# Optimization experiments

Measured on AMD Instinct MI355X. Metric: run time of the kernel, lower is better.

## Reference

```python
import jax, jax.numpy as jnp
from jax import lax
import numpy as np

DIM = 768        # d_model (mamba-130m)
D_IN = 1024      # vision encoder feature dim
NQ = 384         # num_queries
NB = 12          # num_blocks
BATCH = 2
LSEQ = 1024      # image tokens
DI = 2 * DIM     # mamba d_inner (expand=2)
DS = 16          # d_state
DC = 4           # d_conv
DTR = 48         # dt_rank = ceil(768/16)
NH = 16          # attention heads
HD = DIM // NH
NM = NB + 2      # mamba instances: fwd-enc, bwd-enc, one per block


def _ln(x, g, b):
    m = jnp.mean(x, -1, keepdims=True)
    v = jnp.mean((x - m) ** 2, -1, keepdims=True)
    return (x - m) * lax.rsqrt(v + 1e-5) * g + b


def _mamba(x, in_w, conv_w, conv_b, xproj_w, dt_w, dt_b, A_log, Dp, out_w):
    # x: (B, L, DIM)
    Bb = x.shape[0]
    xz = x @ in_w.T                      # (B, L, 2*DI)
    xi, z = jnp.split(xz, 2, -1)
    # depthwise causal conv1d over time
    xc = lax.conv_general_dilated(xi.transpose(0, 2, 1), conv_w[:, None, :], (1,),
                                  [(DC - 1, 0)], feature_group_count=DI,
                                  dimension_numbers=('NCH', 'OIH', 'NCH'))
    xc = jax.nn.silu((xc + conv_b[None, :, None]).transpose(0, 2, 1))  # (B, L, DI)
    dbl = xc @ xproj_w.T                 # (B, L, DTR + 2*DS)
    dt, Bm, Cm = jnp.split(dbl, [DTR, DTR + DS], -1)
    dt = jax.nn.softplus(dt @ dt_w.T + dt_b)   # (B, L, DI)
    A = -jnp.exp(A_log)                        # (DI, DS)
    dA = jnp.exp(dt[..., None] * A)            # (B, L, DI, DS)
    dBx = dt[..., None] * Bm[:, :, None, :] * xc[..., None]

    def step(h, inp):
        dA_t, dBx_t, C_t = inp
        h = dA_t * h + dBx_t
        return h, jnp.einsum('bds,bs->bd', h, C_t)

    h0 = jnp.zeros((Bb, DI, DS), x.dtype)
    _, ys = lax.scan(step, h0, (dA.transpose(1, 0, 2, 3), dBx.transpose(1, 0, 2, 3), Cm.transpose(1, 0, 2)))
    y = ys.transpose(1, 0, 2) + Dp * xc
    y = y * jax.nn.silu(z)
    return y @ out_w.T


def _local_allowed(nq, nk):
    # matches Attention.get_local_mask: query i attends to its contiguous key block
    kpq, extra = nk // nq, nk % nq
    i = jnp.arange(nq)
    start = i * kpq + jnp.minimum(i, extra)
    end = start + kpq + (i < extra)
    k = jnp.arange(nk)
    return (k[None, :] >= start[:, None]) & (k[None, :] < end[:, None])


def _mha(q_in, kv, in_w, in_b, out_w, out_b, allowed):
    # nn.MultiheadAttention(dim, 16, batch_first=True) cross-attention
    wq, wk, wv = jnp.split(in_w, 3, 0)
    bq, bk, bv = jnp.split(in_b, 3, 0)
    Bb = q_in.shape[0]
    q = (q_in @ wq.T + bq).reshape(Bb, -1, NH, HD)
    k = (kv @ wk.T + bk).reshape(Bb, -1, NH, HD)
    v = (kv @ wv.T + bv).reshape(Bb, -1, NH, HD)
    s = jnp.einsum('bqhd,bkhd->bhqk', q, k) / np.float32(np.sqrt(HD))
    s = jnp.where(allowed[None, None], s, -jnp.inf)
    a = jax.nn.softmax(s, -1)
    o = jnp.einsum('bhqk,bkhd->bqhd', a, v).reshape(Bb, -1, DIM)
    return o @ out_w.T + out_b


def _model(img_emb, queries, vision_proj_w, vision_proj_b, ln_vision_g, ln_vision_b,
           mamba_in_w, mamba_conv_w, mamba_conv_b, mamba_xproj_w, mamba_dt_w, mamba_dt_b,
           mamba_A_log, mamba_D, mamba_out_w, seq_norm_g, seq_norm_b,
           attn_in_w, attn_in_b, attn_out_w, attn_out_b, cross_w, cross_b):
    mp = lambda i: (mamba_in_w[i], mamba_conv_w[i], mamba_conv_b[i], mamba_xproj_w[i],
                    mamba_dt_w[i], mamba_dt_b[i], mamba_A_log[i], mamba_D[i], mamba_out_w[i])
    feats = _ln(img_emb @ vision_proj_w.T + vision_proj_b, ln_vision_g, ln_vision_b)
    fwd = _mamba(feats, *mp(0))
    bwd = jnp.flip(_mamba(jnp.flip(feats, 1), *mp(1)), 1)
    c = fwd + bwd + feats
    x = jnp.broadcast_to(queries, (img_emb.shape[0], NQ, DIM))
    allowed = _local_allowed(NQ, c.shape[1])
    for l in range(NB):
        x = _ln(x, seq_norm_g[l], seq_norm_b[l])
        x = _mamba(x, *mp(l + 2)) + x
        score = _mha(x, c, attn_in_w[l], attn_in_b[l], attn_out_w[l], attn_out_b[l], allowed)
        x = jnp.concatenate([x, score], -1) @ cross_w[l].T + cross_b[l]
    return x


_model_jit = jax.jit(_model)


def setup_inputs() -> dict:
    key = jax.random.key(0)
    ks = iter(jax.random.split(key, 24))
    rn = lambda shape, s=0.02: jax.random.normal(next(ks), shape, jnp.float32) * s
    A_log = jnp.broadcast_to(jnp.log(jnp.arange(1, DS + 1, dtype=jnp.float32)), (NM, DI, DS))
    return {
        'img_emb': rn((BATCH, LSEQ, D_IN), 1.0),
        'queries': rn((1, NQ, DIM)),
        'vision_proj_w': rn((DIM, D_IN)),
        'vision_proj_b': jnp.zeros((DIM,), jnp.float32),
        'ln_vision_g': jnp.ones((DIM,), jnp.float32),
        'ln_vision_b': jnp.zeros((DIM,), jnp.float32),
        'mamba_in_w': rn((NM, 2 * DI, DIM)),
        'mamba_conv_w': rn((NM, DI, DC), 0.1),
        'mamba_conv_b': jnp.zeros((NM, DI), jnp.float32),
        'mamba_xproj_w': rn((NM, DTR + 2 * DS, DI)),
        'mamba_dt_w': rn((NM, DI, DTR), 0.1),
        'mamba_dt_b': rn((NM, DI), 0.5),
        'mamba_A_log': A_log,
        'mamba_D': jnp.ones((NM, DI), jnp.float32),
        'mamba_out_w': rn((NM, DIM, DI)),
        'seq_norm_g': jnp.ones((NB, DIM), jnp.float32),
        'seq_norm_b': jnp.zeros((NB, DIM), jnp.float32),
        'attn_in_w': rn((NB, 3 * DIM, DIM)),
        'attn_in_b': jnp.zeros((NB, 3 * DIM), jnp.float32),
        'attn_out_w': rn((NB, DIM, DIM)),
        'attn_out_b': jnp.zeros((NB, DIM), jnp.float32),
        'cross_w': rn((NB, DIM, 2 * DIM)),
        'cross_b': jnp.zeros((NB, DIM), jnp.float32),
    }


def reference(img_emb, queries, vision_proj_w, vision_proj_b, ln_vision_g, ln_vision_b,
              mamba_in_w, mamba_conv_w, mamba_conv_b, mamba_xproj_w, mamba_dt_w, mamba_dt_b,
              mamba_A_log, mamba_D, mamba_out_w, seq_norm_g, seq_norm_b,
              attn_in_w, attn_in_b, attn_out_w, attn_out_b, cross_w, cross_b):
    return _model_jit(img_emb, queries, vision_proj_w, vision_proj_b, ln_vision_g, ln_vision_b,
                      mamba_in_w, mamba_conv_w, mamba_conv_b, mamba_xproj_w, mamba_dt_w, mamba_dt_b,
                      mamba_A_log, mamba_D, mamba_out_w, seq_norm_g, seq_norm_b,
                      attn_in_w, attn_in_b, attn_out_w, attn_out_b, cross_w, cross_b)
```

## Files before the change

kernel.cpp:

```cpp
#include <hip/hip_runtime.h>
#include <hip/hip_bf16.h>

#define DIMQ 768
#define D_IN 1024
#define NQ 384
#define NBK 12
#define BATCH 2
#define LSEQ 1024
#define DI 1536
#define DS 16
#define DTR 48
#define NH 16
#define HD 48

typedef __attribute__((ext_vector_type(8))) short short8;
typedef __attribute__((ext_vector_type(4))) float f32x4;

#define GF_BIAS 1
#define GF_SOFTPLUS 2
#define EPI_BIAS 1
#define EPI_ADDT 2

#define LOG2E 1.4426950408889634f

__device__ __forceinline__ unsigned short f2bf(float f) {
    unsigned int u = __builtin_bit_cast(unsigned int, f);
    u = (u + 0x7FFFu + ((u >> 16) & 1u)) >> 16;
    return (unsigned short)u;
}
__device__ __forceinline__ float bf2f(unsigned short h) {
    unsigned int u = ((unsigned int)h) << 16;
    return __builtin_bit_cast(float, u);
}

__device__ __forceinline__ void gload_lds16(const void* g, void* l) {
    __builtin_amdgcn_global_load_lds(
        (const __attribute__((address_space(1))) void*)g,
        (__attribute__((address_space(3))) void*)l, 16, 0, 0);
}

struct WTab {
    const float* src[10];
    long long dstOff[10];
    long long ps[10];
    int cum[10];
    int rows[10], cols[10], dcols[10];
    int n;
    int total;
};

__global__ void wconv_kernel(unsigned short* __restrict__ dst, WTab T)
{
    const int i = blockIdx.x * 256 + threadIdx.x;
    if (i >= T.total) return;
    int sI = 0;
    while (i >= T.cum[sI]) ++sI;
    const int e = i - (sI ? T.cum[sI - 1] : 0);
    const int dcols = T.dcols[sI];
    const int r = e / dcols;
    const int c = e - r * dcols;
    float v = 0.f;
    if (r < T.rows[sI] && c < T.cols[sI]) v = T.src[sI][(long long)r * T.cols[sI] + c];
    const unsigned short h = f2bf(v);
    const unsigned short l = f2bf(v - bf2f(h));
    dst[T.dstOff[sI] + e] = h;
    dst[T.dstOff[sI] + T.ps[sI] + e] = l;
}

struct LTab {
    const float* src[7];
    long long srcStride[7], dstOff[7], ps[7];
    int rows[7], cols[7], dcols[7], cum[7];
};

__global__ __launch_bounds__(256)
void wconv_layers(unsigned short* __restrict__ dst, long long layerStride, int lBase, LTab T)
{
    const int e = blockIdx.x * 256 + threadIdx.x;
    const int l = blockIdx.y + lBase;
    int sI = 0;
    while (e >= T.cum[sI]) ++sI;
    const int eo = e - (sI ? T.cum[sI - 1] : 0);
    const int dc = T.dcols[sI];
    const int r = eo / dc;
    const int c = eo - r * dc;
    float v = 0.f;
    if (r < T.rows[sI] && c < T.cols[sI])
        v = T.src[sI][(long long)l * T.srcStride[sI] + (long long)r * T.cols[sI] + c];
    const unsigned short h = f2bf(v);
    const unsigned short lo2 = f2bf(v - bf2f(h));
    unsigned short* d = dst + (long long)blockIdx.y * layerStride + T.dstOff[sI];
    d[eo] = h;
    d[T.ps[sI] + eo] = lo2;
}

__global__ __launch_bounds__(256, 3)
void gemm_direct(const float* __restrict__ Ag, const unsigned short* __restrict__ Bhl,
                 float* __restrict__ Cg, const float* __restrict__ biasg,
                 int M, int N, int K, int lda, int ldb, int ldc,
                 long long sA, long long sB, long long sC, long long sBias,
                 long long planeB, int flags)
{
    __shared__ __align__(16) unsigned short As[2][2][64][40];
    __shared__ __align__(16) unsigned short Bs[2][2][128][32];

    const int z = blockIdx.z;
    const float* A = Ag + (size_t)z * sA;
    const unsigned short* Bhi = Bhl + (size_t)z * sB;
    const unsigned short* Blo = Bhi + planeB;
    float* C = Cg + (size_t)z * sC;

    const int mBase = blockIdx.x * 64;
    const int nBase = blockIdx.y * 128;
    const int tid = threadIdx.x, lane = tid & 63, wave = tid >> 6;
    const int lm = lane & 15, lq = lane >> 4;
    const int wn = wave * 32;
    const int arow = tid >> 2, aq = tid & 3;
    const int brow = lane >> 2;
    const int bcol = (lane & 3) * 8;

    const int ktiles = (K + 31) >> 5;

    auto issueB = [&](int t, int buf) {
#pragma unroll
        for (int cc = 0; cc < 4; ++cc) {
            const int chunk = wave * 4 + cc;
            const int pl = chunk >> 3;
            const int r16 = chunk & 7;
            const unsigned short* bp = pl ? Blo : Bhi;
            const int n = nBase + r16 * 16 + brow;
            gload_lds16(bp + (size_t)n * ldb + t * 32 + bcol, &Bs[buf][pl][r16 * 16][0]);
        }
    };
    auto loadA = [&](int t, float* v) {
        const int col = t * 32 + aq * 8;
        const float* src = A + (size_t)(mBase + arow) * lda + col;
#pragma unroll
        for (int u = 0; u < 2; ++u) {
            float4 t4 = make_float4(0.f, 0.f, 0.f, 0.f);
            if (col + u * 4 < K) t4 = *(const float4*)(src + u * 4);
            v[u*4+0]=t4.x; v[u*4+1]=t4.y; v[u*4+2]=t4.z; v[u*4+3]=t4.w;
        }
    };
    auto writeA = [&](const float* v, int buf) {
        short8 ph, plv;
#pragma unroll
        for (int j = 0; j < 8; ++j) {
            unsigned short h = f2bf(v[j]);
            ph[j] = (short)h;
            plv[j] = (short)f2bf(v[j] - bf2f(h));
        }
        *(short8*)&As[buf][0][arow][aq * 8] = ph;
        *(short8*)&As[buf][1][arow][aq * 8] = plv;
    };

    float av[8];
    issueB(0, 0);
    loadA(0, av);
    writeA(av, 0);

    f32x4 acc[4][2] = {};
    for (int t = 0; t < ktiles; ++t) {
        const int buf = t & 1;
        __syncthreads();
        const bool more = (t + 1) < ktiles;
        if (more) { issueB(t + 1, buf ^ 1); loadA(t + 1, av); }
        short8 ah[4], al[4], bh[2], bl[2];
#pragma unroll
        for (int i = 0; i < 4; ++i) {
            ah[i] = *(const short8*)&As[buf][0][16*i + lm][lq * 8];
            al[i] = *(const short8*)&As[buf][1][16*i + lm][lq * 8];
        }
#pragma unroll
        for (int j = 0; j < 2; ++j) {
            bh[j] = *(const short8*)&Bs[buf][0][wn + 16*j + lm][lq * 8];
            bl[j] = *(const short8*)&Bs[buf][1][wn + 16*j + lm][lq * 8];
        }
#pragma unroll
        for (int i = 0; i < 4; ++i)
#pragma unroll
            for (int j = 0; j < 2; ++j) {
                acc[i][j] = __builtin_amdgcn_mfma_f32_16x16x32_bf16(ah[i], bh[j], acc[i][j], 0, 0, 0);
                acc[i][j] = __builtin_amdgcn_mfma_f32_16x16x32_bf16(ah[i], bl[j], acc[i][j], 0, 0, 0);
                acc[i][j] = __builtin_amdgcn_mfma_f32_16x16x32_bf16(al[i], bh[j], acc[i][j], 0, 0, 0);
            }
        if (more) writeA(av, buf ^ 1);
    }

#pragma unroll
    for (int i = 0; i < 4; ++i)
#pragma unroll
        for (int j = 0; j < 2; ++j)
#pragma unroll
            for (int r = 0; r < 4; ++r) {
                const int m = mBase + i*16 + lq*4 + r;
                const int n = nBase + wn + j*16 + lm;
                float v = acc[i][j][r];
                if (flags & GF_BIAS)     v += biasg[(size_t)z * sBias + n];
                if (flags & GF_SOFTPLUS) v = (v > 20.f) ? v : log1pf(expf(v));
                C[(size_t)m * ldc + n] = v;
            }
}

__global__ __launch_bounds__(256, 3)
void gemm_splitk(const float* __restrict__ Ag, const unsigned short* __restrict__ Bhl,
                 float* __restrict__ Cp,
                 int M, int kLen, int S, int lda, int ldb, int ldP,
                 long long sA, long long sB, long long planeB)
{
    __shared__ __align__(16) unsigned short As[2][2][64][40];
    __shared__ __align__(16) unsigned short Bs[2][2][128][32];

    const int bz = blockIdx.z;
    const int s = bz % S, z = bz / S;
    const int kOff = s * kLen;
    const float* A = Ag + (size_t)z * sA;
    const unsigned short* Bhi = Bhl + (size_t)z * sB;
    const unsigned short* Blo = Bhi + planeB;

    const int mBase = blockIdx.x * 64;
    const int nBase = blockIdx.y * 128;
    const int tid = threadIdx.x, lane = tid & 63, wave = tid >> 6;
    const int lm = lane & 15, lq = lane >> 4;
    const int wn = wave * 32;
    const int arow = tid >> 2, aq = tid & 3;
    const int brow = lane >> 2;
    const int bcol = (lane & 3) * 8;

    const int ktiles = kLen >> 5;

    auto issueB = [&](int t, int buf) {
#pragma unroll
        for (int cc = 0; cc < 4; ++cc) {
            const int chunk = wave * 4 + cc;
            const int pl = chunk >> 3;
            const int r16 = chunk & 7;
            const unsigned short* bp = pl ? Blo : Bhi;
            const int n = nBase + r16 * 16 + brow;
            gload_lds16(bp + (size_t)n * ldb + kOff + t * 32 + bcol, &Bs[buf][pl][r16 * 16][0]);
        }
    };
    auto loadA = [&](int t, float* v) {
        const float* src = A + (size_t)(mBase + arow) * lda + kOff + t * 32 + aq * 8;
#pragma unroll
        for (int u = 0; u < 2; ++u) {
            const float4 t4 = *(const float4*)(src + u * 4);
            v[u*4+0]=t4.x; v[u*4+1]=t4.y; v[u*4+2]=t4.z; v[u*4+3]=t4.w;
        }
    };
    auto writeA = [&](const float* v, int buf) {
        short8 ph, plv;
#pragma unroll
        for (int j = 0; j < 8; ++j) {
            unsigned short h = f2bf(v[j]);
            ph[j] = (short)h;
            plv[j] = (short)f2bf(v[j] - bf2f(h));
        }
        *(short8*)&As[buf][0][arow][aq * 8] = ph;
        *(short8*)&As[buf][1][arow][aq * 8] = plv;
    };

    float av[8];
    issueB(0, 0);
    loadA(0, av);
    writeA(av, 0);

    f32x4 acc[4][2] = {};
    for (int t = 0; t < ktiles; ++t) {
        const int buf = t & 1;
        __syncthreads();
        const bool more = (t + 1) < ktiles;
        if (more) { issueB(t + 1, buf ^ 1); loadA(t + 1, av); }
        short8 ah[4], al[4], bh[2], bl[2];
#pragma unroll
        for (int i = 0; i < 4; ++i) {
            ah[i] = *(const short8*)&As[buf][0][16*i + lm][lq * 8];
            al[i] = *(const short8*)&As[buf][1][16*i + lm][lq * 8];
        }
#pragma unroll
        for (int j = 0; j < 2; ++j) {
            bh[j] = *(const short8*)&Bs[buf][0][wn + 16*j + lm][lq * 8];
            bl[j] = *(const short8*)&Bs[buf][1][wn + 16*j + lm][lq * 8];
        }
#pragma unroll
        for (int i = 0; i < 4; ++i)
#pragma unroll
            for (int j = 0; j < 2; ++j) {
                acc[i][j] = __builtin_amdgcn_mfma_f32_16x16x32_bf16(ah[i], bh[j], acc[i][j], 0, 0, 0);
                acc[i][j] = __builtin_amdgcn_mfma_f32_16x16x32_bf16(ah[i], bl[j], acc[i][j], 0, 0, 0);
                acc[i][j] = __builtin_amdgcn_mfma_f32_16x16x32_bf16(al[i], bh[j], acc[i][j], 0, 0, 0);
            }
        if (more) writeA(av, buf ^ 1);
    }

    float* Cb = Cp + (size_t)bz * M * ldP;
#pragma unroll
    for (int i = 0; i < 4; ++i)
#pragma unroll
        for (int j = 0; j < 2; ++j)
#pragma unroll
            for (int r = 0; r < 4; ++r) {
                const int m = mBase + i*16 + lq*4 + r;
                const int n = nBase + wn + j*16 + lm;
                Cb[(size_t)m * ldP + n] = acc[i][j][r];
            }
}

__global__ void epi_kernel(const float* __restrict__ Cp, float* __restrict__ outF,
                           const float* __restrict__ bias, const float* __restrict__ addT,
                           int Z, int S, int M, int N, int ldP, int ldOut,
                           long long sOutZ, long long sBiasZ, int ldAdd, int flags)
{
    const int n4 = N >> 2;
    const int idx = blockIdx.x * 256 + threadIdx.x;
    if (idx >= Z * M * n4) return;
    const int c4 = idx % n4;
    const int rem = idx / n4;
    const int m = rem % M;
    const int z = rem / M;
    const int n = c4 * 4;
    const float* base = Cp + ((size_t)z * S * M + m) * ldP + n;
    float4 v = *(const float4*)base;
    for (int s = 1; s < S; ++s) {
        const float4 u = *(const float4*)(base + (size_t)s * M * ldP);
        v.x += u.x; v.y += u.y; v.z += u.z; v.w += u.w;
    }
    if (flags & EPI_BIAS) {
        const float4 b4 = *(const float4*)(bias + (size_t)z * sBiasZ + n);
        v.x += b4.x; v.y += b4.y; v.z += b4.z; v.w += b4.w;
    }
    if (flags & EPI_ADDT) {
        const float4 a4 = *(const float4*)(addT + (size_t)m * ldAdd + n);
        v.x += a4.x; v.y += a4.y; v.z += a4.z; v.w += a4.w;
    }
    *(float4*)(outF + (size_t)z * sOutZ + (size_t)m * ldOut + n) = v;
}

__global__ void ln_kernel(const float* __restrict__ in, float* __restrict__ out,
                          const float* __restrict__ g, const float* __restrict__ b,
                          int rows, int srcMod)
{
    const int row = blockIdx.x * 4 + (threadIdx.x >> 6);
    const int lane = threadIdx.x & 63;
    if (row >= rows) return;
    const float* p = in + (size_t)(row % srcMod) * DIMQ;
    float v[12], s = 0.f, s2 = 0.f;
#pragma unroll
    for (int j = 0; j < 12; ++j) {
        v[j] = p[j*64 + lane];
        s += v[j];
        s2 += v[j]*v[j];
    }
#pragma unroll
    for (int o = 32; o; o >>= 1) { s += __shfl_xor(s, o); s2 += __shfl_xor(s2, o); }
    const float mean = s * (1.f/768.f);
    const float var  = s2 * (1.f/768.f) - mean*mean;
    const float inv  = rsqrtf(var + 1e-5f);
    float* q = out + (size_t)row * DIMQ;
#pragma unroll
    for (int j = 0; j < 12; ++j) {
        const int c = j*64 + lane;
        q[c] = (v[j] - mean) * inv * g[c] + b[c];
    }
}

__global__ void conv_kernel(const float* __restrict__ xz, float* __restrict__ xc,
                            const float* __restrict__ cw, const float* __restrict__ cb,
                            int Bn, int L, int instShift)
{
    const int idx = blockIdx.x * 256 + threadIdx.x;
    const int total = Bn * L * (DI/4);
    if (idx >= total) return;
    const int d4 = idx % (DI/4);
    const int t  = (idx / (DI/4)) % L;
    const int b  = idx / (L * (DI/4));
    const int inst = b >> instShift;
    const int d = d4 * 4;
    const float* base = xz + (size_t)(b * L) * 3072 + d;
    const float4 w0 = *(const float4*)(cw + (size_t)(inst*DI + d + 0) * 4);
    const float4 w1 = *(const float4*)(cw + (size_t)(inst*DI + d + 1) * 4);
    const float4 w2 = *(const float4*)(cw + (size_t)(inst*DI + d + 2) * 4);
    const float4 w3 = *(const float4*)(cw + (size_t)(inst*DI + d + 3) * 4);
    float4 acc = *(const float4*)(cb + (size_t)inst*DI + d);
    float4 xv[4];
#pragma unroll
    for (int j = 0; j < 4; ++j) {
        const int tt = t - 3 + j;
        xv[j] = (tt >= 0) ? *(const float4*)(base + (size_t)tt * 3072) : make_float4(0,0,0,0);
    }
    acc.x += xv[0].x*w0.x + xv[1].x*w0.y + xv[2].x*w0.z + xv[3].x*w0.w;
    acc.y += xv[0].y*w1.x + xv[1].y*w1.y + xv[2].y*w1.z + xv[3].y*w1.w;
    acc.z += xv[0].z*w2.x + xv[1].z*w2.y + xv[2].z*w2.z + xv[3].z*w2.w;
    acc.w += xv[0].w*w3.x + xv[1].w*w3.y + xv[2].w*w3.z + xv[3].w*w3.w;
    float4 o;
    o.x = acc.x / (1.f + expf(-acc.x));
    o.y = acc.y / (1.f + expf(-acc.y));
    o.z = acc.z / (1.f + expf(-acc.z));
    o.w = acc.w / (1.f + expf(-acc.w));
    *(float4*)(xc + (size_t)(b * L + t) * DI + d) = o;
}

__global__ __launch_bounds__(256)
void scan_p1(const float* __restrict__ dt, const float* __restrict__ dbl,
             const float* __restrict__ xc, const float* __restrict__ A_log,
             float* __restrict__ hend, float* __restrict__ sumdt,
             int L, int CL, int Bn, int instShift)
{
    const int d = blockIdx.x * 256 + threadIdx.x;
    const int b = blockIdx.y;
    const int c = blockIdx.z;
    const int inst = b >> instShift;
    const float* ap = A_log + ((size_t)inst * DI + d) * DS;
    float A2[16];
#pragma unroll
    for (int s = 0; s < 16; ++s) A2[s] = -expf(ap[s]) * LOG2E;
    float h[16] = {};
    float sd = 0.f;
    const int t0 = c * CL;
    const size_t rowbase = (size_t)b * L;
    for (int t = t0; t < t0 + CL; ++t) {
        const size_t row = rowbase + t;
        const float dtv = dt[row * DI + d];
        const float xcv = xc[row * DI + d];
        float Bv[16];
        *(float4*)(Bv + 0)  = *(const float4*)(dbl + row * 80 + 48);
        *(float4*)(Bv + 4)  = *(const float4*)(dbl + row * 80 + 52);
        *(float4*)(Bv + 8)  = *(const float4*)(dbl + row * 80 + 56);
        *(float4*)(Bv + 12) = *(const float4*)(dbl + row * 80 + 60);
        sd += dtv;
        const float bx = dtv * xcv;
#pragma unroll
        for (int s = 0; s < 16; ++s)
            h[s] = exp2f(dtv * A2[s]) * h[s] + bx * Bv[s];
    }
    float* hp = hend + (((size_t)c * Bn + b) * DI + d) * DS;
#pragma unroll
    for (int s = 0; s < 16; s += 4)
        *(float4*)(hp + s) = make_float4(h[s], h[s+1], h[s+2], h[s+3]);
    sumdt[((size_t)c * Bn + b) * DI + d] = sd;
}

__global__ void scan_p2(const float* __restrict__ hend, const float* __restrict__ sumdt,
                        const float* __restrict__ A_log, float* __restrict__ hstart,
                        int NC, int Bn, int instShift)
{
    const int gid = blockIdx.x * 256 + threadIdx.x;
    const int s = gid & 15;
    const int rem = gid >> 4;
    const int d = rem % DI;
    const int b = rem / DI;
    const int inst = b >> instShift;
    const float A2 = -expf(A_log[((size_t)inst * DI + d) * DS + s]) * LOG2E;
    float carry = 0.f;
    for (int c = 0; c < NC; ++c) {
        const size_t off = (((size_t)c * Bn + b) * DI + d) * DS + s;
        hstart[off] = carry;
        carry = exp2f(A2 * sumdt[((size_t)c * Bn + b) * DI + d]) * carry + hend[off];
    }
}

__global__ __launch_bounds__(256)
void scan_p3(const float* __restrict__ dt, const float* __restrict__ dbl,
             const float* __restrict__ xc, const float* __restrict__ xz,
             const float* __restrict__ A_log, const float* __restrict__ Dp,
             const float* __restrict__ hstart, float* __restrict__ y,
             int L, int CL, int Bn, int instShift)
{
    const int d = blockIdx.x * 256 + threadIdx.x;
    const int b = blockIdx.y;
    const int c = blockIdx.z;
    const int inst = b >> instShift;
    const float* ap = A_log + ((size_t)inst * DI + d) * DS;
    float A2[16];
#pragma unroll
    for (int s = 0; s < 16; ++s) A2[s] = -expf(ap[s]) * LOG2E;
    const float Dd = Dp[(size_t)inst * DI + d];
    float h[16];
    const float* hp = hstart + (((size_t)c * Bn + b) * DI + d) * DS;
#pragma unroll
    for (int s = 0; s < 16; s += 4) {
        const float4 t4 = *(const float4*)(hp + s);
        h[s] = t4.x; h[s+1] = t4.y; h[s+2] = t4.z; h[s+3] = t4.w;
    }
    const int t0 = c * CL;
    const size_t rowbase = (size_t)b * L;
    for (int t = t0; t < t0 + CL; ++t) {
        const size_t row = rowbase + t;
        const float dtv = dt[row * DI + d];
        const float xcv = xc[row * DI + d];
        const float zv  = xz[row * 3072 + DI + d];
        float Bv[16], Cv[16];
        *(float4*)(Bv + 0)  = *(const float4*)(dbl + row * 80 + 48);
        *(float4*)(Bv + 4)  = *(const float4*)(dbl + row * 80 + 52);
        *(float4*)(Bv + 8)  = *(const float4*)(dbl + row * 80 + 56);
        *(float4*)(Bv + 12) = *(const float4*)(dbl + row * 80 + 60);
        *(float4*)(Cv + 0)  = *(const float4*)(dbl + row * 80 + 64);
        *(float4*)(Cv + 4)  = *(const float4*)(dbl + row * 80 + 68);
        *(float4*)(Cv + 8)  = *(const float4*)(dbl + row * 80 + 72);
        *(float4*)(Cv + 12) = *(const float4*)(dbl + row * 80 + 76);
        const float bx = dtv * xcv;
#pragma unroll
        for (int s = 0; s < 16; ++s)
            h[s] = exp2f(dtv * A2[s]) * h[s] + bx * Bv[s];
        float p0 = 0.f, p1 = 0.f, p2 = 0.f, p3 = 0.f;
#pragma unroll
        for (int s = 0; s < 4; ++s) {
            p0 += h[s]      * Cv[s];
            p1 += h[s + 4]  * Cv[s + 4];
            p2 += h[s + 8]  * Cv[s + 8];
            p3 += h[s + 12] * Cv[s + 12];
        }
        const float p = (p0 + p1) + (p2 + p3);
        y[row * DI + d] = (p + Dd * xcv) * (zv / (1.f + expf(-zv)));
    }
}

__global__ void attn_kernel(const float* __restrict__ q, const float* __restrict__ kv,
                            float* __restrict__ o)
{
    const int bi = blockIdx.x;
    const int b = bi / NQ, i = bi % NQ;
    const int tid = threadIdx.x;
    const int h = tid >> 2, r = tid & 3;
    int start, len;
    if (i < 256) { start = 3*i; len = 3; } else { start = 2*i + 256; len = 2; }
    const float* qp = q + (size_t)bi * DIMQ + h*48 + r*12;
    float qv[12];
#pragma unroll
    for (int u = 0; u < 12; ++u) qv[u] = qp[u];
    float s[3] = {-1e30f, -1e30f, -1e30f};
    for (int j = 0; j < len; ++j) {
        const float* kp = kv + (size_t)(b*LSEQ + start + j) * 1536 + h*48 + r*12;
        float p = 0.f;
#pragma unroll
        for (int u = 0; u < 12; ++u) p += qv[u] * kp[u];
        p += __shfl_xor(p, 1);
        p += __shfl_xor(p, 2);
        s[j] = p * 0.14433756729740644f;
    }
    const float mx = fmaxf(s[0], fmaxf(s[1], s[2]));
    float e[3];
    e[0] = expf(s[0]-mx); e[1] = expf(s[1]-mx); e[2] = expf(s[2]-mx);
    const float inv = 1.f / (e[0] + e[1] + e[2]);
    float ov[12] = {};
    for (int j = 0; j < len; ++j) {
        const float w = e[j] * inv;
        const float* vp = kv + (size_t)(b*LSEQ + start + j) * 1536 + 768 + h*48 + r*12;
#pragma unroll
        for (int u = 0; u < 12; ++u) ov[u] += w * vp[u];
    }
    float* op = o + (size_t)bi * DIMQ + h*48 + r*12;
#pragma unroll
    for (int u = 0; u < 12; ++u) op[u] = ov[u];
}

__global__ void flip_kernel(float* __restrict__ X2)
{
    const int idx = blockIdx.x * 256 + threadIdx.x;
    if (idx >= 2*1024*192) return;
    const int d4 = idx % 192;
    const int t  = (idx / 192) % 1024;
    const int b  = idx / (192 * 1024);
    const size_t dst = ((size_t)((2+b)*1024 + t)) * DIMQ + d4*4;
    const size_t src = ((size_t)(b*1024 + (1023 - t))) * DIMQ + d4*4;
    *(float4*)(X2 + dst) = *(const float4*)(X2 + src);
}

__global__ void combine_kernel(const float* __restrict__ oe, const float* __restrict__ feats,
                               float* __restrict__ c)
{
    const int idx = blockIdx.x * 256 + threadIdx.x;
    if (idx >= 2*1024*192) return;
    const int d4 = idx % 192;
    const int t  = (idx / 192) % 1024;
    const int b  = idx / (192 * 1024);
    const size_t fw = ((size_t)(b*1024 + t)) * DIMQ + d4*4;
    const size_t bw = ((size_t)((2+b)*1024 + (1023 - t))) * DIMQ + d4*4;
    const float4 a = *(const float4*)(oe + fw);
    const float4 bb = *(const float4*)(oe + bw);
    const float4 f = *(const float4*)(feats + fw);
    float4 o;
    o.x = a.x + bb.x + f.x; o.y = a.y + bb.y + f.y;
    o.z = a.z + bb.z + f.z; o.w = a.w + bb.w + f.w;
    *(float4*)(c + fw) = o;
}

extern "C" void kernel_launch(void* const* d_in, const int* in_sizes, int n_in,
                              void* d_out, int out_size, void* d_ws, size_t ws_size,
                              hipStream_t stream) {
    const float* img_emb  = (const float*)d_in[0];
    const float* queries  = (const float*)d_in[1];
    const float* vis_w    = (const float*)d_in[2];
    const float* vis_b    = (const float*)d_in[3];
    const float* lnv_g    = (const float*)d_in[4];
    const float* lnv_b    = (const float*)d_in[5];
    const float* m_in_w   = (const float*)d_in[6];
    const float* m_conv_w = (const float*)d_in[7];
    const float* m_conv_b = (const float*)d_in[8];
    const float* m_xp_w   = (const float*)d_in[9];
    const float* m_dt_w   = (const float*)d_in[10];
    const float* m_dt_b   = (const float*)d_in[11];
    const float* m_A_log  = (const float*)d_in[12];
    const float* m_D      = (const float*)d_in[13];
    const float* m_out_w  = (const float*)d_in[14];
    const float* sn_g     = (const float*)d_in[15];
    const float* sn_b     = (const float*)d_in[16];
    const float* a_in_w   = (const float*)d_in[17];
    const float* a_in_b   = (const float*)d_in[18];
    const float* a_out_w  = (const float*)d_in[19];
    const float* a_out_b  = (const float*)d_in[20];
    const float* cr_w     = (const float*)d_in[21];
    const float* cr_b     = (const float*)d_in[22];
    float* out = (float*)d_out;

    float* ws = (float*)d_ws;
    auto alloc = [&](size_t n) { float* p = ws; ws += n; return p; };
    float* X2   = alloc((size_t)4096*768);
    float* xzb  = alloc((size_t)4096*3072);
    float* xcb  = alloc((size_t)4096*1536);
    float* dblb = alloc((size_t)4096*80);
    float* dtb  = alloc((size_t)4096*1536);
    float* yb   = alloc((size_t)4096*1536);
    float* oe   = alloc((size_t)4096*768);
    float* cbuf = alloc((size_t)2048*768);
    float* xbuf = alloc((size_t)768*768);
    float* xn   = alloc((size_t)768*768);
    float* x1s  = alloc((size_t)768*1536);
    float* qb   = alloc((size_t)768*768);
    float* ob   = alloc((size_t)768*768);
    float* Cp   = alloc((size_t)2359296);
    unsigned short* wenc = (unsigned short*)alloc((size_t)16908288/2);

    const long long LAYER_USH = 14745600;
    const size_t usedFloats = (size_t)(ws - (float*)d_ws);
    const size_t needFull = (usedFloats + (size_t)12 * (LAYER_USH/2)) * 4;
    const bool bigW = ws_size >= needFull;
    unsigned short* wlayAll = (unsigned short*)ws;

    const long long P_VIS = 768LL*1024;
    const long long P_IN  = 3072LL*768;
    const long long P_XP  = 128LL*1536;
    const long long P_DT  = 1536LL*64;
    const long long P_OUT = 768LL*1536;
    const long long P_AIN = 2304LL*768;
    const long long P_AOUT= 768LL*768;
    const long long P_CR  = 768LL*1536;
    const long long off_vis   = 0;
    const long long off_encIn = 2*P_VIS;
    const long long off_encXp = off_encIn + 4*P_IN;
    const long long off_encDt = off_encXp + 4*P_XP;
    const long long off_encOut= off_encDt + 4*P_DT;
    const long long off_in  = 0;
    const long long off_xp  = 2*P_IN;
    const long long off_dt  = off_xp + 2*P_XP;
    const long long off_out = off_dt + 2*P_DT;
    const long long off_aIn = off_out + 2*P_OUT;
    const long long off_aOut= off_aIn + 2*P_AIN;
    const long long off_cr  = off_aOut + 2*P_AOUT;

    auto addSeg = [](WTab& T, const float* src, int rows, int cols, int drows, int dcols,
                     long long dstOff) {
        const int k = T.n;
        T.src[k] = src; T.rows[k] = rows; T.cols[k] = cols; T.dcols[k] = dcols;
        T.ps[k] = (long long)drows * dcols;
        T.dstOff[k] = dstOff;
        T.total += drows * dcols;
        T.cum[k] = T.total;
        T.n = k + 1;
    };

    auto GD = [&](const float* A, const unsigned short* Bhl, long long planeB,
                  float* C, const float* bias,
                  int M, int N, int K, int lda, int ldb, int ldc,
                  long long sA, long long sB, long long sC, long long sBias,
                  int Z, int flags) {
        dim3 grid(M/64, N/128, Z);
        gemm_direct<<<grid, 256, 0, stream>>>(A, Bhl, C, bias, M, N, K, lda, ldb, ldc,
                                              sA, sB, sC, sBias, planeB, flags);
    };
    auto GS = [&](const float* A, const unsigned short* Bhl, long long planeB,
                  int M, int Ntile, int kLen, int S, int lda, int ldb, int ldP,
                  long long sA, long long sB, int Z) {
        dim3 grid(M/64, Ntile/128, Z*S);
        gemm_splitk<<<grid, 256, 0, stream>>>(A, Bhl, Cp, M, kLen, S, lda, ldb, ldP,
                                              sA, sB, planeB);
    };
    auto EPI = [&](float* outF, const float* bias, const float* addT,
                   int Z, int S, int M, int N, int ldP, int ldOut,
                   long long sOutZ, long long sBiasZ, int ldAdd, int flags) {
        const int total = Z * M * (N/4);
        epi_kernel<<<(total+255)/256, 256, 0, stream>>>(Cp, outF, bias, addT, Z, S, M, N,
                                                        ldP, ldOut, sOutZ, sBiasZ, ldAdd, flags);
    };

    {
        WTab T = {}; T.n = 0; T.total = 0;
        addSeg(T, vis_w, 768, 1024, 768, 1024, off_vis);
        addSeg(T, m_in_w,               3072, 768, 3072, 768, off_encIn);
        addSeg(T, m_in_w + 3072*768,    3072, 768, 3072, 768, off_encIn + 2*P_IN);
        addSeg(T, m_xp_w,               80, 1536, 128, 1536, off_encXp);
        addSeg(T, m_xp_w + 80*1536,     80, 1536, 128, 1536, off_encXp + 2*P_XP);
        addSeg(T, m_dt_w,               1536, 48, 1536, 64, off_encDt);
        addSeg(T, m_dt_w + 1536*48,     1536, 48, 1536, 64, off_encDt + 2*P_DT);
        addSeg(T, m_out_w,              768, 1536, 768, 1536, off_encOut);
        addSeg(T, m_out_w + 768*1536,   768, 1536, 768, 1536, off_encOut + 2*P_OUT);
        wconv_kernel<<<(T.total+255)/256, 256, 0, stream>>>(wenc, T);
    }

    LTab LT = {};
    {
        auto seg = [&](int k, const float* src, long long srcStride, int rows, int cols,
                       int drows, int dcols, long long dstOff) {
            LT.src[k] = src; LT.srcStride[k] = srcStride;
            LT.rows[k] = rows; LT.cols[k] = cols; LT.dcols[k] = dcols;
            LT.ps[k] = (long long)drows * dcols; LT.dstOff[k] = dstOff;
            LT.cum[k] = (k ? LT.cum[k-1] : 0) + drows * dcols;
        };
        seg(0, m_in_w  + (size_t)2*3072*768, 3072LL*768, 3072, 768, 3072, 768, off_in);
        seg(1, m_xp_w  + (size_t)2*80*1536,  80LL*1536,  80, 1536, 128, 1536, off_xp);
        seg(2, m_dt_w  + (size_t)2*1536*48,  1536LL*48,  1536, 48, 1536, 64, off_dt);
        seg(3, m_out_w + (size_t)2*768*1536, 768LL*1536, 768, 1536, 768, 1536, off_out);
        seg(4, a_in_w,  2304LL*768, 2304, 768, 2304, 768, off_aIn);
        seg(5, a_out_w, 768LL*768,  768, 768, 768, 768, off_aOut);
        seg(6, cr_w,    768LL*1536, 768, 1536, 768, 1536, off_cr);
    }
    if (bigW)
        wconv_layers<<<dim3(28800, 12), 256, 0, stream>>>(wlayAll, LAYER_USH, 0, LT);

    GD(img_emb, wenc + off_vis, P_VIS, oe, vis_b,
       2048, 768, 1024, 1024, 1024, 768, 0,0,0,0, 1, GF_BIAS);
    ln_kernel<<<512, 256, 0, stream>>>(oe, X2, lnv_g, lnv_b, 2048, 2048);
    flip_kernel<<<(2*1024*192 + 255)/256, 256, 0, stream>>>(X2);

    GD(X2, wenc + off_encIn, P_IN, xzb, nullptr,
       2048, 3072, 768, 768, 768, 3072, 2048LL*768, 2*P_IN, 2048LL*3072, 0, 2, 0);
    conv_kernel<<<(4*1024*384 + 255)/256, 256, 0, stream>>>(xzb, xcb, m_conv_w, m_conv_b, 4, 1024, 1);
    GS(xcb, wenc + off_encXp, P_XP, 2048, 128, 384, 4, 1536, 1536, 128,
       2048LL*1536, 2*P_XP, 2);
    EPI(dblb, nullptr, nullptr, 2, 4, 2048, 80, 128, 80, 2048LL*80, 0, 0, 0);
    GD(dblb, wenc + off_encDt, P_DT, dtb, m_dt_b,
       2048, 1536, 48, 80, 64, 1536, 2048LL*80, 2*P_DT, 2048LL*1536, 1536, 2,
       GF_BIAS | GF_SOFTPLUS);
    {
        const int NC = 16, CL = 64;
        float* hend   = oe;
        float* hstart = oe + (size_t)NC*4*DI*DS;
        float* sumdt  = cbuf;
        scan_p1<<<dim3(6, 4, NC), 256, 0, stream>>>(dtb, dblb, xcb, m_A_log, hend, sumdt, 1024, CL, 4, 1);
        scan_p2<<<(4*DI*DS)/256, 256, 0, stream>>>(hend, sumdt, m_A_log, hstart, NC, 4, 1);
        scan_p3<<<dim3(6, 4, NC), 256, 0, stream>>>(dtb, dblb, xcb, xzb, m_A_log, m_D, hstart, yb, 1024, CL, 4, 1);
    }
    GD(yb, wenc + off_encOut, P_OUT, oe, nullptr,
       2048, 768, 1536, 1536, 1536, 768, 2048LL*1536, 2*P_OUT, 2048LL*768, 0, 2, 0);
    combine_kernel<<<(2*1024*192 + 255)/256, 256, 0, stream>>>(oe, X2, cbuf);

    for (int l = 0; l < NBK; ++l) {
        const int li = l + 2;
        const unsigned short* wl = bigW ? wlayAll + (size_t)l * LAYER_USH : wlayAll;
        if (!bigW)
            wconv_layers<<<dim3(28800, 1), 256, 0, stream>>>((unsigned short*)wlayAll, LAYER_USH, l, LT);

        ln_kernel<<<192, 256, 0, stream>>>(l == 0 ? queries : xbuf, xn,
                                           sn_g + (size_t)l*768, sn_b + (size_t)l*768,
                                           768, l == 0 ? 384 : 768);
        GD(xn, wl + off_in, P_IN, xzb, nullptr,
           768, 3072, 768, 768, 768, 3072, 0,0,0,0, 1, 0);
        conv_kernel<<<(2*NQ*384 + 255)/256, 256, 0, stream>>>(
            xzb, xcb, m_conv_w + (size_t)li*DI*4, m_conv_b + (size_t)li*DI, 2, NQ, 8);
        GS(xcb, wl + off_xp, P_XP, 768, 128, 96, 16, 1536, 1536, 128, 0, 0, 1);
        EPI(dblb, nullptr, nullptr, 1, 16, 768, 80, 128, 80, 0, 0, 0, 0);
        GD(dblb, wl + off_dt, P_DT, dtb, m_dt_b + (size_t)li*1536,
           768, 1536, 48, 80, 64, 1536, 0,0,0,0, 1, GF_BIAS | GF_SOFTPLUS);
        {
            const int NC = 24, CL = 16;
            const float* Ap = m_A_log + (size_t)li*DI*DS;
            float* hend   = oe;
            float* hstart = oe + (size_t)NC*2*DI*DS;
            float* sumdt  = oe + (size_t)2*NC*2*DI*DS;
            scan_p1<<<dim3(6, 2, NC), 256, 0, stream>>>(dtb, dblb, xcb, Ap, hend, sumdt, NQ, CL, 2, 8);
            scan_p2<<<(2*DI*DS)/256, 256, 0, stream>>>(hend, sumdt, Ap, hstart, NC, 2, 8);
            scan_p3<<<dim3(6, 2, NC), 256, 0, stream>>>(dtb, dblb, xcb, xzb, Ap, m_D + (size_t)li*DI,
                                                        hstart, yb, NQ, CL, 2, 8);
        }
        GS(yb, wl + off_out, P_OUT, 768, 768, 384, 4, 1536, 1536, 768, 0, 0, 1);
        EPI(x1s, nullptr, xn, 1, 4, 768, 768, 768, 1536, 0, 0, 768, EPI_ADDT);
        GS(x1s, wl + off_aIn, P_AIN, 768, 768, 192, 4, 1536, 768, 768, 0, 0, 1);
        EPI(qb, a_in_b + (size_t)l*2304, nullptr, 1, 4, 768, 768, 768, 768, 0, 0, 0, EPI_BIAS);
        GD(cbuf, wl + off_aIn + 768LL*768, P_AIN, oe, a_in_b + (size_t)l*2304 + 768,
           2048, 1536, 768, 768, 768, 1536, 0,0,0,0, 1, GF_BIAS);
        attn_kernel<<<2*NQ, 64, 0, stream>>>(qb, oe, ob);
        GS(ob, wl + off_aOut, P_AOUT, 768, 768, 192, 4, 768, 768, 768, 0, 0, 1);
        EPI(x1s + 768, a_out_b + (size_t)l*768, nullptr, 1, 4, 768, 768, 768, 1536, 0, 0, 0, EPI_BIAS);
        float* dst = (l == NBK - 1) ? out : xbuf;
        GS(x1s, wl + off_cr, P_CR, 768, 768, 384, 4, 1536, 1536, 768, 0, 0, 1);
        EPI(dst, cr_b + (size_t)l*768, nullptr, 1, 4, 768, 768, 768, 768, 0, 0, 0, EPI_BIAS);
    }
}
```

Baseline: 4.189 ms.

## Hoist per-layer cross-attn K/V projection into one batched GEMM; fuse epilogue with LN

The K/V projection of the encoder context depends only on the encoder output and the per-layer weights, so all 12 layers' K/V are now computed up front in a single batched GEMM when the workspace is large enough. Separately, the cross-projection split-K epilogue is fused with the next layer's LayerNorm in a new per-row kernel, which removes the separate LN launch and the intermediate xbuf round trip. This trades about 150MB of extra workspace for fewer launches and better GEMM occupancy. The new LN computes variance as E[x^2]-mean^2 in fp32, which differs slightly numerically from the two-pass version.

```diff
diff --git a/kernel.cpp b/kernel.cpp
--- a/kernel.cpp
+++ b/kernel.cpp
@@ -334,6 +334,43 @@
         v.x += a4.x; v.y += a4.y; v.z += a4.z; v.w += a4.w;
     }
     *(float4*)(outF + (size_t)z * sOutZ + (size_t)m * ldOut + n) = v;
+}
+
+__global__ __launch_bounds__(256)
+void epi_ln_kernel(const float* __restrict__ Cp, float* __restrict__ outF,
+                   const float* __restrict__ bias,
+                   const float* __restrict__ g, const float* __restrict__ b,
+                   int S, int M, int ldP)
+{
+    const int m = blockIdx.x;
+    const int tid = threadIdx.x;
+    __shared__ float red[8];
+    float v[3];
+    float s = 0.f, s2 = 0.f;
+#pragma unroll
+    for (int j = 0; j < 3; ++j) {
+        const int n = tid + j * 256;
+        const float* pp = Cp + (size_t)m * ldP + n;
+        float x = pp[0];
+        for (int q = 1; q < S; ++q) x += pp[(size_t)q * M * ldP];
+        x += bias[n];
+        v[j] = x; s += x; s2 += x * x;
+    }
+#pragma unroll
+    for (int o = 32; o; o >>= 1) { s += __shfl_xor(s, o); s2 += __shfl_xor(s2, o); }
+    const int wv = tid >> 6;
+    if ((tid & 63) == 0) { red[wv] = s; red[4 + wv] = s2; }
+    __syncthreads();
+    s  = red[0] + red[1] + red[2] + red[3];
+    s2 = red[4] + red[5] + red[6] + red[7];
+    const float mean = s * (1.f/768.f);
+    const float var  = s2 * (1.f/768.f) - mean * mean;
+    const float inv  = rsqrtf(var + 1e-5f);
+#pragma unroll
+    for (int j = 0; j < 3; ++j) {
+        const int n = tid + j * 256;
+        outF[(size_t)m * DIMQ + n] = (v[j] - mean) * inv * g[n] + b[n];
+    }
 }
 
 __global__ void ln_kernel(const float* __restrict__ in, float* __restrict__ out,
@@ -623,7 +660,6 @@
     float* yb   = alloc((size_t)4096*1536);
     float* oe   = alloc((size_t)4096*768);
     float* cbuf = alloc((size_t)2048*768);
-    float* xbuf = alloc((size_t)768*768);
     float* xn   = alloc((size_t)768*768);
     float* x1s  = alloc((size_t)768*1536);
     float* qb   = alloc((size_t)768*768);
@@ -636,6 +672,11 @@
     const size_t needFull = (usedFloats + (size_t)12 * (LAYER_USH/2)) * 4;
     const bool bigW = ws_size >= needFull;
     unsigned short* wlayAll = (unsigned short*)ws;
+
+    const size_t kvFloats = (size_t)12 * 2048 * 1536;
+    const size_t needKV = needFull + kvFloats * 4;
+    const bool kvHoist = bigW && ws_size >= needKV;
+    float* kvAll = (float*)(wlayAll + (size_t)12 * LAYER_USH);
 
     const long long P_VIS = 768LL*1024;
     const long long P_IN  = 3072LL*768;
@@ -754,15 +795,19 @@
        2048, 768, 1536, 1536, 1536, 768, 2048LL*1536, 2*P_OUT, 2048LL*768, 0, 2, 0);
     combine_kernel<<<(2*1024*192 + 255)/256, 256, 0, stream>>>(oe, X2, cbuf);
 
+    if (kvHoist)
+        GD(cbuf, wlayAll + off_aIn + 768LL*768, P_AIN, kvAll, a_in_b + 768,
+           2048, 1536, 768, 768, 768, 1536,
+           0, LAYER_USH, 2048LL*1536, 2304, 12, GF_BIAS);
+
+    ln_kernel<<<192, 256, 0, stream>>>(queries, xn, sn_g, sn_b, 768, 384);
+
     for (int l = 0; l < NBK; ++l) {
         const int li = l + 2;
         const unsigned short* wl = bigW ? wlayAll + (size_t)l * LAYER_USH : wlayAll;
         if (!bigW)
             wconv_layers<<<dim3(28800, 1), 256, 0, stream>>>((unsigned short*)wlayAll, LAYER_USH, l, LT);
 
-        ln_kernel<<<192, 256, 0, stream>>>(l == 0 ? queries : xbuf, xn,
-                                           sn_g + (size_t)l*768, sn_b + (size_t)l*768,
-                                           768, l == 0 ? 384 : 768);
         GD(xn, wl + off_in, P_IN, xzb, nullptr,
            768, 3072, 768, 768, 768, 3072, 0,0,0,0, 1, 0);
         conv_kernel<<<(2*NQ*384 + 255)/256, 256, 0, stream>>>(
@@ -786,13 +831,25 @@
         EPI(x1s, nullptr, xn, 1, 4, 768, 768, 768, 1536, 0, 0, 768, EPI_ADDT);
         GS(x1s, wl + off_aIn, P_AIN, 768, 768, 192, 4, 1536, 768, 768, 0, 0, 1);
         EPI(qb, a_in_b + (size_t)l*2304, nullptr, 1, 4, 768, 768, 768, 768, 0, 0, 0, EPI_BIAS);
-        GD(cbuf, wl + off_aIn + 768LL*768, P_AIN, oe, a_in_b + (size_t)l*2304 + 768,
-           2048, 1536, 768, 768, 768, 1536, 0,0,0,0, 1, GF_BIAS);
-        attn_kernel<<<2*NQ, 64, 0, stream>>>(qb, oe, ob);
+        const float* kvp;
+        if (kvHoist) {
+            kvp = kvAll + (size_t)l * 2048 * 1536;
+        } else {
+            GD(cbuf, wl + off_aIn + 768LL*768, P_AIN, oe, a_in_b + (size_t)l*2304 + 768,
+               2048, 1536, 768, 768, 768, 1536, 0,0,0,0, 1, GF_BIAS);
+            kvp = oe;
+        }
+        attn_kernel<<<2*NQ, 64, 0, stream>>>(qb, kvp, ob);
         GS(ob, wl + off_aOut, P_AOUT, 768, 768, 192, 4, 768, 768, 768, 0, 0, 1);
         EPI(x1s + 768, a_out_b + (size_t)l*768, nullptr, 1, 4, 768, 768, 768, 1536, 0, 0, 0, EPI_BIAS);
-        float* dst = (l == NBK - 1) ? out : xbuf;
         GS(x1s, wl + off_cr, P_CR, 768, 768, 384, 4, 1536, 1536, 768, 0, 0, 1);
-        EPI(dst, cr_b + (size_t)l*768, nullptr, 1, 4, 768, 768, 768, 768, 0, 0, 0, EPI_BIAS);
-    }
-}
+        if (l == NBK - 1) {
+            EPI(out, cr_b + (size_t)l*768, nullptr, 1, 4, 768, 768, 768, 768, 0, 0, 0, EPI_BIAS);
+        } else {
+            epi_ln_kernel<<<768, 256, 0, stream>>>(Cp, xn, cr_b + (size_t)l*768,
+                                                   sn_g + (size_t)(l+1)*768,
+                                                   sn_b + (size_t)(l+1)*768,
+                                                   4, 768, 768);
+        }
+    }
+}
```

Measured after the change: 4.160 ms. No clear change (-0.7%).
